# Kernel optimization log

Measured on AMD Instinct MI355X. Metric: run time of the kernel, lower is better.

Reference implementation:

```python
import jax, jax.numpy as jnp
import numpy as np

B, T, N, D = 16, 12, 512, 64
ED, EDS, HS, HT, NUM_ROUTE = 32, 32, 16, 32, 3
TT = HS * T

def squash(x, axis=-1):
    sq = jnp.sum(x * x, axis=axis, keepdims=True)
    return (sq / (1.0 + sq)) * x / (jnp.sqrt(sq) + 1e-08)

def lrelu(x):
    return jnp.where(x >= 0, x, 0.01 * x)

def setup_inputs() -> dict:
    key = jax.random.key(0)
    ks = jax.random.split(key, 10)
    u = lambda k, s: jax.random.uniform(k, s, jnp.float32, -0.1, 0.1)
    return {
        'x': jax.random.normal(ks[0], (B, T, N, D), jnp.float32),
        'node_embeddings': u(ks[1], (N, ED)),
        'time_eb': jax.random.normal(ks[2], (B, EDS), jnp.float32),
        'teb': jax.random.normal(ks[3], (B, T, EDS), jnp.float32),
        'W_p': u(ks[4], (D, D)),
        'b_p': u(ks[5], (D,)),
        't_adj': u(ks[6], (EDS, HT, TT)),
        'adj': u(ks[7], (EDS, HS, N)),
        'weights_spa': u(ks[8], (ED, D, D)),
        'bias_spa': u(ks[9], (ED, D)),
    }

def reference(x, node_embeddings, time_eb, teb, W_p, b_p, t_adj, adj, weights_spa, bias_spa):
    # primary capsules
    Pc = squash(x @ W_p + b_p)                                   # [B,T,N,D]
    # dynamic spatial hyper-adjacency
    dadj = jnp.einsum('btd,dhn->bthn', teb, adj)                 # [B,T,HS,N]
    test1 = jnp.einsum('bthn,btnd->bthd', jax.nn.softmax(dadj, axis=2), Pc)
    # u_hat[b,t,h,n,d] = squash(test1)[b,t,h,d] * Pc[b,t,n,d] (detached in routing)
    u_hat = jax.lax.stop_gradient(jnp.einsum('bthd,btnd->bthnd', squash(test1), Pc))
    k = jax.lax.stop_gradient(Pc)
    # dynamic routing (fixed small num_route iterations)
    b_log = jnp.zeros((B, T, HS, N), x.dtype)
    for _ in range(NUM_ROUTE):
        c = jax.nn.softmax(b_log, axis=2)                        # over HS
        s = jnp.einsum('bthn,bthnd->bthd', c, u_hat)
        v = squash(s)
        b_log = b_log + jnp.einsum('bthd,btnd->bthn', v, k)
    c = jax.nn.softmax(b_log + dadj, axis=2)                     # [B,T,HS,N]
    s = jnp.einsum('bthn,btnd->bthd', c, Pc)                     # [B,T,HS,D]
    mask_template = jnp.linspace(1.0, T, T) / 12.0               # [T]
    hyper_spa = (s + mask_template[None, :, None, None]).reshape(B, TT, D)
    # temporal hypergraph aggregation
    dyn = jnp.einsum('bd,dhk->bhk', time_eb, t_adj)              # [B,HT,TT]
    hyper_tem = lrelu(jnp.einsum('bhk,bkd->bhd', dyn, hyper_spa))
    ret_tem = lrelu(jnp.einsum('bhk,bhd->bkd', dyn, hyper_tem))  # [B,TT,D]
    v = squash(ret_tem.reshape(B, T, HS, D) + s)
    # reconstruction back to nodes
    recon = jnp.einsum('bthn,bthd->btnd', c, v)                  # [B,T,N,D]
    W_spatial = jnp.einsum('nd,dio->nio', node_embeddings, weights_spa)
    b_spatial = node_embeddings @ bias_spa                       # [N,D]
    out = jnp.einsum('btni,nio->btno', recon, W_spatial) + b_spatial
    return (lrelu(out + x),
            jax.lax.stop_gradient(c[..., None]),
            jax.lax.stop_gradient(dyn))
```

## Files before the change

kernel.cpp:

```cpp
#include <hip/hip_runtime.h>
#include <hip/hip_bf16.h>

#define B_ 16
#define T_ 12
#define N_ 512
#define D_ 64
#define EDS_ 32
#define HS_ 16
#define HT_ 32
#define TT_ 192
#define BT_ (B_*T_)

typedef unsigned int uint32;

__device__ __forceinline__ float warp_sum64(float v) {
    #pragma unroll
    for (int off = 32; off > 0; off >>= 1) v += __shfl_xor(v, off);
    return v;
}

__device__ __forceinline__ float squash_factor(float sq) {
    return (sq / (1.f + sq)) / (sqrtf(sq) + 1e-8f);
}

__device__ __forceinline__ float lrelu(float v) {
    return (v >= 0.f) ? v : 0.01f * v;
}

__device__ __forceinline__ float bflo(uint32 p) { return __uint_as_float(p << 16); }
__device__ __forceinline__ float bfhi(uint32 p) { return __uint_as_float(p & 0xffff0000u); }

__device__ __forceinline__ unsigned short f2bf(float f) {
    __hip_bfloat16 b = __float2bfloat16(f);
    return *(unsigned short*)&b;
}

__global__ __launch_bounds__(256) void k_pc(const float* __restrict__ x,
        const float* __restrict__ Wp, const float* __restrict__ bp,
        unsigned short* __restrict__ PcgT) {
    __shared__ float Ws[64][64];
    __shared__ float xs[32][64];
    __shared__ unsigned short tb[32][66];
    int tid = threadIdx.x;
    for (int i = tid; i < 1024; i += 256)
        ((float4*)&Ws[0][0])[i] = ((const float4*)Wp)[i];
    int bt = blockIdx.x >> 4;
    int n0 = (blockIdx.x & 15) * 32;
    size_t row0 = (size_t)bt * 512 + n0;
    const float4* xsrc = (const float4*)(x + row0 * 64);
    for (int i = tid; i < 512; i += 256)
        ((float4*)&xs[0][0])[i] = xsrc[i];
    __syncthreads();
    int r = tid >> 6, d = tid & 63;
    float bpd = bp[d];
    #pragma unroll
    for (int m = 0; m < 8; ++m) {
        int row = r + m * 4;
        float acc = bpd;
        #pragma unroll
        for (int k = 0; k < 64; ++k) acc += xs[row][k] * Ws[k][d];
        float sq = warp_sum64(acc * acc);
        tb[row][d] = f2bf(acc * squash_factor(sq));
    }
    __syncthreads();
    for (int i = tid; i < 1024; i += 256) {
        int dd = i >> 4, np = i & 15;
        uint32 lo = tb[np * 2][dd], hi = tb[np * 2 + 1][dd];
        uint32 pack = lo | (hi << 16);
        *(uint32*)(PcgT + ((size_t)bt * 64 + dd) * 512 + n0 + np * 2) = pack;
    }
}

__global__ __launch_bounds__(256) void k_dyn(const float* __restrict__ time_eb,
        const float* __restrict__ t_adj, float* __restrict__ dyn_out) {
    int b = blockIdx.x / 24;
    int chunk = blockIdx.x - b * 24;
    __shared__ float te[32];
    int tid = threadIdx.x;
    if (tid < 32) te[tid] = time_eb[b * 32 + tid];
    __syncthreads();
    int i = chunk * 256 + tid;
    int ht = i / 192, k = i - ht * 192;
    float acc = 0.f;
    #pragma unroll
    for (int dd = 0; dd < 32; ++dd) acc += te[dd] * t_adj[(dd * 32 + ht) * 192 + k];
    dyn_out[(size_t)b * 6144 + i] = acc;
}

__global__ __launch_bounds__(1024) void k_route2(
        const float* __restrict__ teb, const float* __restrict__ adj,
        const unsigned short* __restrict__ PcgT,
        float* __restrict__ c_out, float* __restrict__ s_out) {
    __shared__ __align__(16) unsigned short PcT[64][514];
    __shared__ __align__(16) float cb[16][512];
    __shared__ __align__(16) float blg[16][512];
    __shared__ __align__(16) float sred[4][16][64];
    __shared__ __align__(16) float sq1b[16][64];
    __shared__ float te[32];
    const int bt = blockIdx.x;
    const int tid = threadIdx.x;

    {
        const uint32* src = (const uint32*)(PcgT + (size_t)bt * 32768);
        uint32* dst = (uint32*)&PcT[0][0];
        #pragma unroll
        for (int i = tid; i < 16384; i += 1024) {
            int dd = i >> 8, k = i & 255;
            dst[dd * 257 + k] = src[i];
        }
    }
    if (tid < 32) te[tid] = teb[bt * 32 + tid];
    for (int i = tid; i < 8192; i += 1024) (&blg[0][0])[i] = 0.f;
    __syncthreads();

    #pragma unroll
    for (int grp = 0; grp < 2; ++grp) {
        int i = (tid + grp * 1024) * 4;
        int h = i >> 9, n0 = i & 511;
        float4 a4 = {0.f, 0.f, 0.f, 0.f};
        #pragma unroll
        for (int dd = 0; dd < 32; ++dd) {
            float4 a = *(const float4*)&adj[(size_t)(dd * 16 + h) * 512 + n0];
            float t = te[dd];
            a4.x = fmaf(t, a.x, a4.x);
            a4.y = fmaf(t, a.y, a4.y);
            a4.z = fmaf(t, a.z, a4.z);
            a4.w = fmaf(t, a.w, a4.w);
        }
        *(float4*)&cb[h][n0] = a4;
    }
    __syncthreads();

    const int na = tid >> 1;
    const int g  = tid & 1;
    const int d  = tid & 63;
    const int seg = (tid >> 6) & 3;
    const int h0 = (tid >> 8) * 4;
    const int hr = tid >> 6;
    float* vb = &sred[0][0][0];

    float dv[8];
    #pragma unroll
    for (int j = 0; j < 8; ++j) dv[j] = cb[g * 8 + j][na];

    for (int it = 0; it < 5; ++it) {
        {
            float vv[8];
            #pragma unroll
            for (int j = 0; j < 8; ++j) {
                float bl = (it == 0) ? 0.f : blg[g * 8 + j][na];
                vv[j] = (it == 0) ? dv[j] : ((it == 4) ? bl + dv[j] : bl);
            }
            float m = vv[0];
            #pragma unroll
            for (int j = 1; j < 8; ++j) m = fmaxf(m, vv[j]);
            m = fmaxf(m, __shfl_xor(m, 1));
            float ssum = 0.f;
            #pragma unroll
            for (int j = 0; j < 8; ++j) { vv[j] = __expf(vv[j] - m); ssum += vv[j]; }
            ssum += __shfl_xor(ssum, 1);
            float inv = 1.f / ssum;
            #pragma unroll
            for (int j = 0; j < 8; ++j) {
                float cv = vv[j] * inv;
                cb[g * 8 + j][na] = cv;
                if (it == 4) c_out[((size_t)bt * 16 + g * 8 + j) * 512 + na] = cv;
            }
        }
        __syncthreads();

        {
            float s4[4] = {0.f, 0.f, 0.f, 0.f};
            const uint32* prow = (const uint32*)&PcT[0][0] + d * 257 + seg * 64;
            #pragma unroll 4
            for (int np = 0; np < 64; np += 2) {
                uint32 pa = prow[np], pb = prow[np + 1];
                float p0 = bflo(pa), p1 = bfhi(pa), p2 = bflo(pb), p3 = bfhi(pb);
                int n0 = seg * 128 + np * 2;
                #pragma unroll
                for (int j = 0; j < 4; ++j) {
                    float4 c4 = *(const float4*)&cb[h0 + j][n0];
                    s4[j] = fmaf(c4.x, p0, fmaf(c4.y, p1, fmaf(c4.z, p2, fmaf(c4.w, p3, s4[j]))));
                }
            }
            #pragma unroll
            for (int j = 0; j < 4; ++j) sred[seg][h0 + j][d] = s4[j];
        }
        __syncthreads();

        {
            float s = sred[0][hr][d] + sred[1][hr][d] + sred[2][hr][d] + sred[3][hr][d];
            if (it == 0) {
                float sq = warp_sum64(s * s);
                sq1b[hr][d] = s * squash_factor(sq);
            } else if (it < 4) {
                float st = sq1b[hr][d] * s;
                float sq = warp_sum64(st * st);
                vb[hr * 64 + d] = st * squash_factor(sq);
            } else {
                s_out[((size_t)bt * 16 + hr) * 64 + d] = s;
            }
        }

        if (it >= 1 && it <= 3) {
            const int w = hr;
            const uint32* pc0 = (const uint32*)&PcT[0][0];
            #pragma unroll
            for (int c4i = 0; c4i < 4; ++c4i) {
                int npair = c4i * 64 + d;
                float b0 = 0.f, b1 = 0.f;
                #pragma unroll 8
                for (int dd = 0; dd < 64; dd += 4) {
                    float4 v4 = *(const float4*)&vb[w * 64 + dd];
                    uint32 q0 = pc0[(dd + 0) * 257 + npair];
                    uint32 q1 = pc0[(dd + 1) * 257 + npair];
                    uint32 q2 = pc0[(dd + 2) * 257 + npair];
                    uint32 q3 = pc0[(dd + 3) * 257 + npair];
                    b0 = fmaf(v4.x, bflo(q0), b0); b1 = fmaf(v4.x, bfhi(q0), b1);
                    b0 = fmaf(v4.y, bflo(q1), b0); b1 = fmaf(v4.y, bfhi(q1), b1);
                    b0 = fmaf(v4.z, bflo(q2), b0); b1 = fmaf(v4.z, bfhi(q2), b1);
                    b0 = fmaf(v4.w, bflo(q3), b0); b1 = fmaf(v4.w, bfhi(q3), b1);
                }
                float2* bp2 = (float2*)&blg[w][0] + npair;
                float2 o = *bp2; o.x += b0; o.y += b1; *bp2 = o;
            }
        }
        __syncthreads();
    }
}

__global__ __launch_bounds__(1024) void k_temporal(const float* __restrict__ dyn_in,
        const float* __restrict__ s_out, float* __restrict__ v2) {
    __shared__ float dyn[32][192];
    __shared__ float sblk[192][64];
    __shared__ float htem[32][64];
    __shared__ float mdot[32];
    int b = blockIdx.x, tid = threadIdx.x;
    const float4* dsrc = (const float4*)(dyn_in + (size_t)b * 6144);
    for (int i = tid; i < 1536; i += 1024) ((float4*)&dyn[0][0])[i] = dsrc[i];
    const float4* ssrc = (const float4*)(s_out + (size_t)b * 12288);
    for (int i = tid; i < 3072; i += 1024) ((float4*)&sblk[0][0])[i] = ssrc[i];
    __syncthreads();
    if (tid < 32) {
        float acc = 0.f;
        for (int k = 0; k < 192; ++k) acc += dyn[tid][k] * ((float)(k >> 4) + 1.f);
        mdot[tid] = acc * (1.f / 12.f);
    }
    __syncthreads();
    {
        int d = tid & 63, htb = tid >> 6;
        #pragma unroll
        for (int m = 0; m < 2; ++m) {
            int h = htb + m * 16;
            float acc = 0.f;
            for (int k = 0; k < 192; ++k) acc += dyn[h][k] * sblk[k][d];
            htem[h][d] = lrelu(acc + mdot[h]);
        }
    }
    __syncthreads();
    {
        int d = tid & 63, kq = tid >> 6;
        for (int k = kq; k < 192; k += 16) {
            float acc = 0.f;
            #pragma unroll
            for (int ht = 0; ht < 32; ++ht) acc += dyn[ht][k] * htem[ht][d];
            float w = lrelu(acc) + sblk[k][d];
            float sq = warp_sum64(w * w);
            v2[((size_t)b * 192 + k) * 64 + d] = w * squash_factor(sq);
        }
    }
}

__global__ __launch_bounds__(256) void k_wsp(const float* __restrict__ ne,
        const float* __restrict__ wspa, const float* __restrict__ bspa,
        float* __restrict__ Wsp, float* __restrict__ bsp) {
    int n = blockIdx.x;
    __shared__ float nes[32];
    int tid = threadIdx.x;
    if (tid < 32) nes[tid] = ne[n * 32 + tid];
    __syncthreads();
    for (int i = tid; i < 4096; i += 256) {
        float acc = 0.f;
        #pragma unroll
        for (int dd = 0; dd < 32; ++dd) acc += nes[dd] * wspa[dd * 4096 + i];
        Wsp[(size_t)n * 4096 + i] = acc;
    }
    if (tid < 64) {
        float acc = 0.f;
        #pragma unroll
        for (int dd = 0; dd < 32; ++dd) acc += nes[dd] * bspa[dd * 64 + tid];
        bsp[n * 64 + tid] = acc;
    }
}

__global__ __launch_bounds__(256) void k_final(const float* __restrict__ c_out,
        const float* __restrict__ v2, const float* __restrict__ Wsp,
        const float* __restrict__ bsp, const float* __restrict__ x,
        float* __restrict__ out) {
    int n = blockIdx.x & 511;
    int gq = blockIdx.x >> 9;
    __shared__ float Ws[64][64];
    __shared__ float rec[4][64];
    int tid = threadIdx.x;
    const float4* wsrc = (const float4*)(Wsp + (size_t)n * 4096);
    for (int i = tid; i < 1024; i += 256) ((float4*)&Ws[0][0])[i] = wsrc[i];
    __syncthreads();
    int r = tid >> 6, o = tid & 63;
    float bias = bsp[n * 64 + o];
    for (int bt0 = gq * 12; bt0 < gq * 12 + 12; bt0 += 4) {
        int bt = bt0 + r;
        float ri = 0.f;
        #pragma unroll
        for (int h = 0; h < 16; ++h)
            ri += c_out[((size_t)bt * 16 + h) * 512 + n] * v2[((size_t)bt * 16 + h) * 64 + o];
        rec[r][o] = ri;
        __syncthreads();
        float acc = bias;
        #pragma unroll
        for (int i = 0; i < 64; ++i) acc += rec[r][i] * Ws[i][o];
        size_t idx = ((size_t)bt * 512 + n) * 64 + o;
        out[idx] = lrelu(acc + x[idx]);
        __syncthreads();
    }
}

extern "C" void kernel_launch(void* const* d_in, const int* in_sizes, int n_in,
                              void* d_out, int out_size, void* d_ws, size_t ws_size,
                              hipStream_t stream) {
    const float* x       = (const float*)d_in[0];
    const float* ne      = (const float*)d_in[1];
    const float* time_eb = (const float*)d_in[2];
    const float* teb     = (const float*)d_in[3];
    const float* Wp      = (const float*)d_in[4];
    const float* bp      = (const float*)d_in[5];
    const float* t_adj   = (const float*)d_in[6];
    const float* adj     = (const float*)d_in[7];
    const float* wspa    = (const float*)d_in[8];
    const float* bspa    = (const float*)d_in[9];

    float* out0    = (float*)d_out;
    float* c_out   = out0 + 6291456;
    float* dyn_out = out0 + 7864320;

    float* ws    = (float*)d_ws;
    float* s_out = ws;
    float* v2    = ws + 196608;
    float* Wsp   = ws + 393216;
    float* bsp   = ws + 2490368;
    unsigned short* PcgT = (unsigned short*)(ws + 2523136);

    k_pc<<<BT_ * 16, 256, 0, stream>>>(x, Wp, bp, PcgT);
    k_wsp<<<N_, 256, 0, stream>>>(ne, wspa, bspa, Wsp, bsp);
    k_dyn<<<B_ * 24, 256, 0, stream>>>(time_eb, t_adj, dyn_out);
    k_route2<<<BT_, 1024, 0, stream>>>(teb, adj, PcgT, c_out, s_out);
    k_temporal<<<B_, 1024, 0, stream>>>(dyn_out, s_out, v2);
    k_final<<<N_ * 16, 256, 0, stream>>>(c_out, v2, Wsp, bsp, x, out0);
}
```

Baseline: 342.5 us.

## Keep routing logits in registers and tile k_wsp over eight nodes

Result: faster. 294.7 us (-14.0%).

```diff
diff --git a/kernel.cpp b/kernel.cpp
--- a/kernel.cpp
+++ b/kernel.cpp
@@ -29,6 +29,9 @@
 
 __device__ __forceinline__ float bflo(uint32 p) { return __uint_as_float(p << 16); }
 __device__ __forceinline__ float bfhi(uint32 p) { return __uint_as_float(p & 0xffff0000u); }
+__device__ __forceinline__ float bf2f(unsigned short u) {
+    return __uint_as_float(((uint32)u) << 16);
+}
 
 __device__ __forceinline__ unsigned short f2bf(float f) {
     __hip_bfloat16 b = __float2bfloat16(f);
@@ -93,7 +96,6 @@
         float* __restrict__ c_out, float* __restrict__ s_out) {
     __shared__ __align__(16) unsigned short PcT[64][514];
     __shared__ __align__(16) float cb[16][512];
-    __shared__ __align__(16) float blg[16][512];
     __shared__ __align__(16) float sred[4][16][64];
     __shared__ __align__(16) float sq1b[16][64];
     __shared__ float te[32];
@@ -110,7 +112,6 @@
         }
     }
     if (tid < 32) te[tid] = teb[bt * 32 + tid];
-    for (int i = tid; i < 8192; i += 1024) (&blg[0][0])[i] = 0.f;
     __syncthreads();
 
     #pragma unroll
@@ -139,18 +140,19 @@
     const int hr = tid >> 6;
     float* vb = &sred[0][0][0];
 
-    float dv[8];
-    #pragma unroll
-    for (int j = 0; j < 8; ++j) dv[j] = cb[g * 8 + j][na];
+    float dv[8], blog[8];
+    #pragma unroll
+    for (int j = 0; j < 8; ++j) {
+        dv[j] = cb[g * 8 + j][na];
+        blog[j] = 0.f;
+    }
 
     for (int it = 0; it < 5; ++it) {
         {
             float vv[8];
             #pragma unroll
-            for (int j = 0; j < 8; ++j) {
-                float bl = (it == 0) ? 0.f : blg[g * 8 + j][na];
-                vv[j] = (it == 0) ? dv[j] : ((it == 4) ? bl + dv[j] : bl);
-            }
+            for (int j = 0; j < 8; ++j)
+                vv[j] = (it == 0) ? dv[j] : ((it == 4) ? blog[j] + dv[j] : blog[j]);
             float m = vv[0];
             #pragma unroll
             for (int j = 1; j < 8; ++j) m = fmaxf(m, vv[j]);
@@ -201,31 +203,25 @@
                 s_out[((size_t)bt * 16 + hr) * 64 + d] = s;
             }
         }
+        __syncthreads();
 
         if (it >= 1 && it <= 3) {
-            const int w = hr;
-            const uint32* pc0 = (const uint32*)&PcT[0][0];
-            #pragma unroll
-            for (int c4i = 0; c4i < 4; ++c4i) {
-                int npair = c4i * 64 + d;
-                float b0 = 0.f, b1 = 0.f;
-                #pragma unroll 8
-                for (int dd = 0; dd < 64; dd += 4) {
-                    float4 v4 = *(const float4*)&vb[w * 64 + dd];
-                    uint32 q0 = pc0[(dd + 0) * 257 + npair];
-                    uint32 q1 = pc0[(dd + 1) * 257 + npair];
-                    uint32 q2 = pc0[(dd + 2) * 257 + npair];
-                    uint32 q3 = pc0[(dd + 3) * 257 + npair];
-                    b0 = fmaf(v4.x, bflo(q0), b0); b1 = fmaf(v4.x, bfhi(q0), b1);
-                    b0 = fmaf(v4.y, bflo(q1), b0); b1 = fmaf(v4.y, bfhi(q1), b1);
-                    b0 = fmaf(v4.z, bflo(q2), b0); b1 = fmaf(v4.z, bfhi(q2), b1);
-                    b0 = fmaf(v4.w, bflo(q3), b0); b1 = fmaf(v4.w, bfhi(q3), b1);
+            float bacc[8] = {0.f,0.f,0.f,0.f,0.f,0.f,0.f,0.f};
+            #pragma unroll 4
+            for (int dd = 0; dd < 64; dd += 4) {
+                float p0 = bf2f(PcT[dd + 0][na]);
+                float p1 = bf2f(PcT[dd + 1][na]);
+                float p2 = bf2f(PcT[dd + 2][na]);
+                float p3 = bf2f(PcT[dd + 3][na]);
+                #pragma unroll
+                for (int j = 0; j < 8; ++j) {
+                    float4 v4 = *(const float4*)&vb[(g * 8 + j) * 64 + dd];
+                    bacc[j] = fmaf(p0, v4.x, fmaf(p1, v4.y, fmaf(p2, v4.z, fmaf(p3, v4.w, bacc[j]))));
                 }
-                float2* bp2 = (float2*)&blg[w][0] + npair;
-                float2 o = *bp2; o.x += b0; o.y += b1; *bp2 = o;
             }
-        }
-        __syncthreads();
+            #pragma unroll
+            for (int j = 0; j < 8; ++j) blog[j] += bacc[j];
+        }
     }
 }
 
@@ -274,22 +270,40 @@
 __global__ __launch_bounds__(256) void k_wsp(const float* __restrict__ ne,
         const float* __restrict__ wspa, const float* __restrict__ bspa,
         float* __restrict__ Wsp, float* __restrict__ bsp) {
-    int n = blockIdx.x;
-    __shared__ float nes[32];
+    __shared__ float nes[8][32];
+    int bid = blockIdx.x;
+    int n0 = (bid >> 2) * 8;
+    int i0 = (bid & 3) * 1024;
     int tid = threadIdx.x;
-    if (tid < 32) nes[tid] = ne[n * 32 + tid];
-    __syncthreads();
-    for (int i = tid; i < 4096; i += 256) {
-        float acc = 0.f;
-        #pragma unroll
-        for (int dd = 0; dd < 32; ++dd) acc += nes[dd] * wspa[dd * 4096 + i];
-        Wsp[(size_t)n * 4096 + i] = acc;
-    }
-    if (tid < 64) {
-        float acc = 0.f;
-        #pragma unroll
-        for (int dd = 0; dd < 32; ++dd) acc += nes[dd] * bspa[dd * 64 + tid];
-        bsp[n * 64 + tid] = acc;
+    nes[tid >> 5][tid & 31] = ne[(n0 + (tid >> 5)) * 32 + (tid & 31)];
+    __syncthreads();
+    int i = i0 + tid * 4;
+    float4 acc[8];
+    #pragma unroll
+    for (int n = 0; n < 8; ++n) acc[n] = make_float4(0.f, 0.f, 0.f, 0.f);
+    #pragma unroll 8
+    for (int dd = 0; dd < 32; ++dd) {
+        float4 w = *(const float4*)&wspa[dd * 4096 + i];
+        #pragma unroll
+        for (int n = 0; n < 8; ++n) {
+            float e = nes[n][dd];
+            acc[n].x = fmaf(e, w.x, acc[n].x);
+            acc[n].y = fmaf(e, w.y, acc[n].y);
+            acc[n].z = fmaf(e, w.z, acc[n].z);
+            acc[n].w = fmaf(e, w.w, acc[n].w);
+        }
+    }
+    #pragma unroll
+    for (int n = 0; n < 8; ++n)
+        *(float4*)&Wsp[(size_t)(n0 + n) * 4096 + i] = acc[n];
+    if ((bid & 3) == 0) {
+        int o = tid & 63;
+        for (int nn = tid >> 6; nn < 8; nn += 4) {
+            float acc2 = 0.f;
+            #pragma unroll
+            for (int dd = 0; dd < 32; ++dd) acc2 += nes[nn][dd] * bspa[dd * 64 + o];
+            bsp[(n0 + nn) * 64 + o] = acc2;
+        }
     }
 }
 
@@ -350,7 +364,7 @@
     unsigned short* PcgT = (unsigned short*)(ws + 2523136);
 
     k_pc<<<BT_ * 16, 256, 0, stream>>>(x, Wp, bp, PcgT);
-    k_wsp<<<N_, 256, 0, stream>>>(ne, wspa, bspa, Wsp, bsp);
+    k_wsp<<<256, 256, 0, stream>>>(ne, wspa, bspa, Wsp, bsp);
     k_dyn<<<B_ * 24, 256, 0, stream>>>(time_eb, t_adj, dyn_out);
     k_route2<<<BT_, 1024, 0, stream>>>(teb, adj, PcgT, c_out, s_out);
     k_temporal<<<B_, 1024, 0, stream>>>(dyn_out, s_out, v2);
```
